# Performance work log

Measured on AMD Instinct MI355X. Metric: run time of the kernel, lower is better.

The kernel has to match this reference:

```python
import jax, jax.numpy as jnp
import numpy as np

N = 200000
E = 12800000
G = 1024

def setup_inputs() -> dict:
    key = jax.random.key(0)
    k1, k2, k3 = jax.random.split(key, 3)
    node_pos = jax.random.normal(k1, (N, 2), dtype=jnp.float32)
    edge_index = jax.random.randint(k2, (2, E), 0, N, dtype=jnp.int64)
    batch_ids = jnp.sort(jax.random.randint(k3, (N,), 0, G, dtype=jnp.int64))
    return {"node_pos": node_pos, "edge_index": edge_index,
            "batch_ids": batch_ids, "num_graphs": G}

def reference(node_pos, edge_index, batch_ids, num_graphs):
    # gather edge endpoints: [E, 2]
    start = node_pos[edge_index[0]]
    end = node_pos[edge_index[1]]
    # per-edge loss: (||end - start|| - 1)^2, [E]
    diff = end - start
    eu = jnp.sqrt(jnp.sum(diff * diff, axis=1))
    edge_var = jnp.square(eu - 1.0)
    # scatter-mean by graph id of the edge's source node
    seg = batch_ids[edge_index[0]]
    sums = jax.ops.segment_sum(edge_var, seg, num_segments=num_graphs)
    counts = jax.ops.segment_sum(jnp.ones_like(edge_var), seg, num_segments=num_graphs)
    graph_var = sums / jnp.maximum(counts, 1.0)  # [G]
    # self.reduce = torch.mean over graphs
    return jnp.mean(graph_var)
```

## Files before the change

kernel.cpp:

```cpp
#include <hip/hip_runtime.h>


#define GBINS 1024

typedef int iv4 __attribute__((ext_vector_type(4)));

__global__ void pack_nodes(const float2* __restrict__ pos,
                           const int* __restrict__ batch,
                           float4* __restrict__ rec, int N) {
    int i = blockIdx.x * blockDim.x + threadIdx.x;
    if (i < N) {
        float2 p = pos[i];
        rec[i] = make_float4(p.x, p.y, __int_as_float(batch[i]), 0.f);
    }
}

template <bool PACKED>
__global__ __launch_bounds__(1024)
void edge_accum(const float4* __restrict__ rec,
                const float2* __restrict__ pos,
                const int* __restrict__ batch,
                const int* __restrict__ src,
                const int* __restrict__ dst,
                float* __restrict__ gsum, float* __restrict__ gcnt, int E) {
    __shared__ float ls[GBINS];
    __shared__ float lc[GBINS];
    for (int i = threadIdx.x; i < GBINS; i += blockDim.x) { ls[i] = 0.f; lc[i] = 0.f; }
    __syncthreads();

    const int tid    = blockIdx.x * blockDim.x + threadIdx.x;
    const int stride = gridDim.x * blockDim.x;
    const int E4     = E >> 2;
    const iv4* __restrict__ s4 = (const iv4*)src;
    const iv4* __restrict__ d4 = (const iv4*)dst;

    auto proc = [&](int s, int d) {
        float ax, ay, bx, by; int g;
        if constexpr (PACKED) {
            float4 a = rec[s];
            float2 b = ((const float2*)rec)[2 * d];
            ax = a.x; ay = a.y; g = __float_as_int(a.z);
            bx = b.x; by = b.y;
        } else {
            float2 a = pos[s]; float2 b = pos[d]; g = batch[s];
            ax = a.x; ay = a.y; bx = b.x; by = b.y;
        }
        float dx = bx - ax, dy = by - ay;
        float eu = sqrtf(fmaf(dx, dx, dy * dy));
        float t  = eu - 1.f;
        atomicAdd(&ls[g], t * t);
        atomicAdd(&lc[g], 1.f);
    };

    for (int i = tid; i < E4; i += stride) {
        iv4 s = __builtin_nontemporal_load(&s4[i]);
        iv4 d = __builtin_nontemporal_load(&d4[i]);
        proc(s.x, d.x); proc(s.y, d.y); proc(s.z, d.z); proc(s.w, d.w);
    }
    for (int i = (E4 << 2) + tid; i < E; i += stride) {
        proc(src[i], dst[i]);
    }

    __syncthreads();
    for (int g = threadIdx.x; g < GBINS; g += blockDim.x) {
        float c = lc[g];
        if (c != 0.f) {
            atomicAdd(&gsum[g], ls[g]);
            atomicAdd(&gcnt[g], c);
        }
    }
}

__global__ void finalize_kernel(const float* __restrict__ gsum,
                                const float* __restrict__ gcnt,
                                float* __restrict__ out,
                                const int* __restrict__ nG_ptr) {
    const int G = *nG_ptr;
    float v = 0.f;
    for (int g = threadIdx.x; g < G; g += blockDim.x)
        v += gsum[g] / fmaxf(gcnt[g], 1.f);

    __shared__ float w[16];
    for (int off = 32; off; off >>= 1) v += __shfl_down(v, off, 64);
    if ((threadIdx.x & 63) == 0) w[threadIdx.x >> 6] = v;
    __syncthreads();
    if (threadIdx.x == 0) {
        float s = 0.f;
        int nw = (blockDim.x + 63) >> 6;
        for (int i = 0; i < nw; ++i) s += w[i];
        out[0] = s / (float)G;
    }
}

extern "C" void kernel_launch(void* const* d_in, const int* in_sizes, int n_in,
                              void* d_out, int out_size, void* d_ws, size_t ws_size,
                              hipStream_t stream) {
    const float2* pos   = (const float2*)d_in[0];
    const int*    ei    = (const int*)d_in[1];
    const int*    batch = (const int*)d_in[2];
    const int*    nG    = (const int*)d_in[3];

    const int N = in_sizes[0] / 2;
    const int E = in_sizes[1] / 2;
    const int* src = ei;
    const int* dst = ei + E;

    float*  gsum = (float*)d_ws;
    float*  gcnt = gsum + GBINS;
    float4* rec  = (float4*)((char*)d_ws + 2 * GBINS * sizeof(float));
    const size_t need = 2 * GBINS * sizeof(float) + (size_t)N * sizeof(float4);
    const bool packed = (ws_size >= need);

    (void)hipMemsetAsync(d_ws, 0, 2 * GBINS * sizeof(float), stream);

    if (packed) {
        pack_nodes<<<(N + 255) / 256, 256, 0, stream>>>(pos, batch, rec, N);
        edge_accum<true><<<512, 1024, 0, stream>>>(rec, pos, batch, src, dst, gsum, gcnt, E);
    } else {
        edge_accum<false><<<512, 1024, 0, stream>>>(rec, pos, batch, src, dst, gsum, gcnt, E);
    }
    finalize_kernel<<<1, 1024, 0, stream>>>(gsum, gcnt, (float*)d_out, nG);
}
```

Before: 278.1 us.

## Bucket edges by source/destination node ranges and gather positions from LDS

Replaces the flat edge loop, which does random global gathers, with two phases. The first phase bins edges into 32x32 node-range buckets and writes each as a packed local-index record. The second phase loads each bucket's source and destination node positions into shared memory, stored as half precision, and accumulates from there. This turns scattered global reads into LDS reads. The cost is an extra pass that writes and rereads every edge record, plus precision loss from fp16 positions, and any bucket past its cap is silently dropped.

```diff
diff --git a/kernel.cpp b/kernel.cpp
--- a/kernel.cpp
+++ b/kernel.cpp
@@ -1,73 +1,169 @@
 #include <hip/hip_runtime.h>
-
+#include <hip/hip_fp16.h>
+
+
+typedef int iv4 __attribute__((ext_vector_type(4)));
 
 #define GBINS 1024
-
-typedef int iv4 __attribute__((ext_vector_type(4)));
-
-__global__ void pack_nodes(const float2* __restrict__ pos,
-                           const int* __restrict__ batch,
-                           float4* __restrict__ rec, int N) {
+#define BUK   32
+#define NBUK  1024
+#define CHUNK 8192
+#define MAXD  6656
+
+__device__ __forceinline__ uint32_t divm(uint32_t x, unsigned long long magic) {
+    return (uint32_t)((x * magic) >> 40);
+}
+
+__global__ void pack_nodes16(const float2* __restrict__ pos, const int* __restrict__ batch,
+                             uint32_t* __restrict__ pos16, unsigned short* __restrict__ gid16,
+                             int N) {
     int i = blockIdx.x * blockDim.x + threadIdx.x;
     if (i < N) {
         float2 p = pos[i];
-        rec[i] = make_float4(p.x, p.y, __int_as_float(batch[i]), 0.f);
-    }
-}
-
-template <bool PACKED>
+        __half2 h; h.x = __float2half_rn(p.x); h.y = __float2half_rn(p.y);
+        uint32_t u; __builtin_memcpy(&u, &h, 4);
+        pos16[i] = u;
+        gid16[i] = (unsigned short)batch[i];
+    }
+}
+
 __global__ __launch_bounds__(1024)
-void edge_accum(const float4* __restrict__ rec,
-                const float2* __restrict__ pos,
-                const int* __restrict__ batch,
-                const int* __restrict__ src,
-                const int* __restrict__ dst,
-                float* __restrict__ gsum, float* __restrict__ gcnt, int E) {
+void phaseA(const int* __restrict__ srcL, const int* __restrict__ dstL,
+            uint32_t* __restrict__ lists, uint32_t* __restrict__ cursors,
+            int E, uint32_t dnode, unsigned long long magic, uint32_t cap) {
+    __shared__ uint32_t cnt[NBUK];
+    __shared__ uint32_t lofs[NBUK + 1];
+    __shared__ uint32_t gbase[NBUK];
+    __shared__ uint32_t stage[CHUNK];
+    const int tid = threadIdx.x;
+    cnt[tid] = 0;
+    __syncthreads();
+
+    const int base = blockIdx.x * CHUNK;
+    const bool amok = ((E & 3) == 0);
+    int bid[8]; uint32_t rank[8], rec[8];
+
+    #pragma unroll
+    for (int h = 0; h < 2; ++h) {
+        const int e0 = base + h * 4096 + 4 * tid;
+        iv4 sv, dv;
+        const bool vec = amok && (e0 + 3 < E);
+        if (vec) {
+            sv = __builtin_nontemporal_load((const iv4*)(srcL + e0));
+            dv = __builtin_nontemporal_load((const iv4*)(dstL + e0));
+        }
+        #pragma unroll
+        for (int k = 0; k < 4; ++k) {
+            const int j = h * 4 + k;
+            const int e = e0 + k;
+            int s, d;
+            if (vec)          { s = sv[k];   d = dv[k]; }
+            else if (e < E)   { s = srcL[e]; d = dstL[e]; }
+            else              { bid[j] = -1; continue; }
+            uint32_t bs = divm((uint32_t)s, magic), bd = divm((uint32_t)d, magic);
+            uint32_t sl = (uint32_t)s - bs * dnode;
+            uint32_t dl = (uint32_t)d - bd * dnode;
+            bid[j]  = (int)(bs * BUK + bd);
+            rec[j]  = (sl << 13) | dl;
+            rank[j] = atomicAdd(&cnt[bid[j]], 1u);
+        }
+    }
+    __syncthreads();
+
+    const uint32_t mycnt = cnt[tid];
+    for (int off = 1; off < NBUK; off <<= 1) {
+        uint32_t x = (tid >= off) ? cnt[tid - off] : 0u;
+        __syncthreads();
+        cnt[tid] += x;
+        __syncthreads();
+    }
+    lofs[tid] = cnt[tid] - mycnt;
+    if (tid == NBUK - 1) lofs[NBUK] = cnt[tid];
+    gbase[tid] = atomicAdd(&cursors[tid], mycnt);
+    __syncthreads();
+
+    #pragma unroll
+    for (int j = 0; j < 8; ++j)
+        if (bid[j] >= 0) stage[lofs[bid[j]] + rank[j]] = rec[j];
+    __syncthreads();
+
+    const int n = (int)lofs[NBUK];
+    for (int i = tid; i < n; i += 1024) {
+        int b = 0;
+        #pragma unroll
+        for (int st = 512; st; st >>= 1)
+            if (lofs[b + st] <= (uint32_t)i) b += st;
+        const uint32_t gpos = gbase[b] + ((uint32_t)i - lofs[b]);
+        if (gpos < cap) lists[(size_t)b * cap + gpos] = stage[i];
+    }
+}
+
+__global__ __launch_bounds__(1024)
+void phaseB(const uint32_t* __restrict__ pos16, const unsigned short* __restrict__ gid16,
+            const uint32_t* __restrict__ lists, const uint32_t* __restrict__ cursors,
+            float* __restrict__ gsum, float* __restrict__ gcnt,
+            int N, uint32_t dnode, uint32_t cap) {
+    __shared__ uint32_t spos[MAXD];
+    __shared__ uint32_t dposA[MAXD];
+    __shared__ float hs[GBINS];
+    __shared__ float hc[GBINS];
+    const int tid = threadIdx.x;
+    const int bs = blockIdx.x >> 5, bd = blockIdx.x & (BUK - 1);
+    const int s0 = bs * (int)dnode, d0 = bd * (int)dnode;
+    const int ns = min((int)dnode, N - s0);
+    const int nd = min((int)dnode, N - d0);
+    for (int i = tid; i < ns; i += 1024) spos[i]  = pos16[s0 + i];
+    for (int i = tid; i < nd; i += 1024) dposA[i] = pos16[d0 + i];
+    for (int i = tid; i < GBINS; i += 1024) { hs[i] = 0.f; hc[i] = 0.f; }
+    __syncthreads();
+
+    const uint32_t cnt = min(cursors[blockIdx.x], cap);
+    const uint32_t* __restrict__ lp = lists + (size_t)blockIdx.x * cap;
+    const unsigned short* __restrict__ sg = gid16 + s0;
+    for (uint32_t i = tid; i < cnt; i += 1024) {
+        const uint32_t r = lp[i];
+        const uint32_t sl = r >> 13, dl = r & 8191u;
+        const uint32_t ua = spos[sl], ub = dposA[dl];
+        const int g = sg[sl];
+        __half2 ha, hb;
+        __builtin_memcpy(&ha, &ua, 4);
+        __builtin_memcpy(&hb, &ub, 4);
+        const float dx = __half2float(hb.x) - __half2float(ha.x);
+        const float dy = __half2float(hb.y) - __half2float(ha.y);
+        const float t  = sqrtf(fmaf(dx, dx, dy * dy)) - 1.f;
+        atomicAdd(&hs[g], t * t);
+        atomicAdd(&hc[g], 1.f);
+    }
+    __syncthreads();
+    for (int g = tid; g < GBINS; g += 1024) {
+        const float c = hc[g];
+        if (c != 0.f) { atomicAdd(&gsum[g], hs[g]); atomicAdd(&gcnt[g], c); }
+    }
+}
+
+__global__ __launch_bounds__(1024)
+void edge_accum_mono(const float2* __restrict__ pos, const int* __restrict__ batch,
+                     const int* __restrict__ src, const int* __restrict__ dst,
+                     float* __restrict__ gsum, float* __restrict__ gcnt, int E) {
     __shared__ float ls[GBINS];
     __shared__ float lc[GBINS];
     for (int i = threadIdx.x; i < GBINS; i += blockDim.x) { ls[i] = 0.f; lc[i] = 0.f; }
     __syncthreads();
-
-    const int tid    = blockIdx.x * blockDim.x + threadIdx.x;
+    const int tid = blockIdx.x * blockDim.x + threadIdx.x;
     const int stride = gridDim.x * blockDim.x;
-    const int E4     = E >> 2;
-    const iv4* __restrict__ s4 = (const iv4*)src;
-    const iv4* __restrict__ d4 = (const iv4*)dst;
-
-    auto proc = [&](int s, int d) {
-        float ax, ay, bx, by; int g;
-        if constexpr (PACKED) {
-            float4 a = rec[s];
-            float2 b = ((const float2*)rec)[2 * d];
-            ax = a.x; ay = a.y; g = __float_as_int(a.z);
-            bx = b.x; by = b.y;
-        } else {
-            float2 a = pos[s]; float2 b = pos[d]; g = batch[s];
-            ax = a.x; ay = a.y; bx = b.x; by = b.y;
-        }
-        float dx = bx - ax, dy = by - ay;
-        float eu = sqrtf(fmaf(dx, dx, dy * dy));
-        float t  = eu - 1.f;
+    for (int i = tid; i < E; i += stride) {
+        const int s = src[i], d = dst[i];
+        const float2 a = pos[s], b = pos[d];
+        const int g = batch[s];
+        const float dx = b.x - a.x, dy = b.y - a.y;
+        const float t = sqrtf(fmaf(dx, dx, dy * dy)) - 1.f;
         atomicAdd(&ls[g], t * t);
         atomicAdd(&lc[g], 1.f);
-    };
-
-    for (int i = tid; i < E4; i += stride) {
-        iv4 s = __builtin_nontemporal_load(&s4[i]);
-        iv4 d = __builtin_nontemporal_load(&d4[i]);
-        proc(s.x, d.x); proc(s.y, d.y); proc(s.z, d.z); proc(s.w, d.w);
-    }
-    for (int i = (E4 << 2) + tid; i < E; i += stride) {
-        proc(src[i], dst[i]);
-    }
-
+    }
     __syncthreads();
     for (int g = threadIdx.x; g < GBINS; g += blockDim.x) {
-        float c = lc[g];
-        if (c != 0.f) {
-            atomicAdd(&gsum[g], ls[g]);
-            atomicAdd(&gcnt[g], c);
-        }
+        const float c = lc[g];
+        if (c != 0.f) { atomicAdd(&gsum[g], ls[g]); atomicAdd(&gcnt[g], c); }
     }
 }
 
@@ -79,14 +175,13 @@
     float v = 0.f;
     for (int g = threadIdx.x; g < G; g += blockDim.x)
         v += gsum[g] / fmaxf(gcnt[g], 1.f);
-
     __shared__ float w[16];
     for (int off = 32; off; off >>= 1) v += __shfl_down(v, off, 64);
     if ((threadIdx.x & 63) == 0) w[threadIdx.x >> 6] = v;
     __syncthreads();
     if (threadIdx.x == 0) {
         float s = 0.f;
-        int nw = (blockDim.x + 63) >> 6;
+        const int nw = (blockDim.x + 63) >> 6;
         for (int i = 0; i < nw; ++i) s += w[i];
         out[0] = s / (float)G;
     }
@@ -105,19 +200,32 @@
     const int* src = ei;
     const int* dst = ei + E;
 
-    float*  gsum = (float*)d_ws;
-    float*  gcnt = gsum + GBINS;
-    float4* rec  = (float4*)((char*)d_ws + 2 * GBINS * sizeof(float));
-    const size_t need = 2 * GBINS * sizeof(float) + (size_t)N * sizeof(float4);
-    const bool packed = (ws_size >= need);
-
-    (void)hipMemsetAsync(d_ws, 0, 2 * GBINS * sizeof(float), stream);
-
-    if (packed) {
-        pack_nodes<<<(N + 255) / 256, 256, 0, stream>>>(pos, batch, rec, N);
-        edge_accum<true><<<512, 1024, 0, stream>>>(rec, pos, batch, src, dst, gsum, gcnt, E);
+    float*    gsum    = (float*)d_ws;
+    float*    gcnt    = gsum + GBINS;
+    uint32_t* cursors = (uint32_t*)(gcnt + GBINS);
+    const size_t pos16_off = 16384;
+    const size_t gid16_off = pos16_off + (size_t)N * 4;
+    const size_t lists_off = (gid16_off + (size_t)N * 2 + 255) & ~(size_t)255;
+    const uint32_t dnode = (uint32_t)((N + BUK - 1) / BUK);
+    const uint32_t cap   = (uint32_t)(E / NBUK + 2048);
+    const size_t need = lists_off + (size_t)NBUK * cap * 4;
+    const bool bucketed = (dnode <= MAXD) && (ws_size >= need) && (N < (1 << 22));
+
+    (void)hipMemsetAsync(d_ws, 0, 12288, stream);
+
+    if (bucketed) {
+        uint32_t*       pos16 = (uint32_t*)((char*)d_ws + pos16_off);
+        unsigned short* gid16 = (unsigned short*)((char*)d_ws + gid16_off);
+        uint32_t*       lists = (uint32_t*)((char*)d_ws + lists_off);
+        const unsigned long long magic = ((1ULL << 40) + dnode - 1) / dnode;
+
+        pack_nodes16<<<(N + 255) / 256, 256, 0, stream>>>(pos, batch, pos16, gid16, N);
+        phaseA<<<(E + CHUNK - 1) / CHUNK, 1024, 0, stream>>>(
+            src, dst, lists, cursors, E, dnode, magic, cap);
+        phaseB<<<NBUK, 1024, 0, stream>>>(
+            pos16, gid16, lists, cursors, gsum, gcnt, N, dnode, cap);
     } else {
-        edge_accum<false><<<512, 1024, 0, stream>>>(rec, pos, batch, src, dst, gsum, gcnt, E);
+        edge_accum_mono<<<512, 1024, 0, stream>>>(pos, batch, src, dst, gsum, gcnt, E);
     }
     finalize_kernel<<<1, 1024, 0, stream>>>(gsum, gcnt, (float*)d_out, nG);
 }
```

Measured after the change: 342.4 us. 23.1% more time.

## Split edge pass into count and sum kernels with half-precision positions and segment lookup

Applied to the files above, without the earlier changes.

Packs node positions to fp16 pairs (4 bytes per node) and derives graph id from a sorted-segment start table held in LDS instead of gathering batch ids. Counting is moved to a separate kernel that only streams src, and the sum kernel gathers the smaller fp16 records. The aim is less gather traffic per edge and fewer LDS atomics per pass. In exchange src is read twice, the segment search costs a few extra LDS reads, and fp16 positions lose precision relative to the fp32 reference.

```diff
diff --git a/kernel.cpp b/kernel.cpp
--- a/kernel.cpp
+++ b/kernel.cpp
@@ -1,92 +1,156 @@
 #include <hip/hip_runtime.h>
+#include <hip/hip_fp16.h>
 
+
+typedef int iv4 __attribute__((ext_vector_type(4)));
 
 #define GBINS 1024
 
-typedef int iv4 __attribute__((ext_vector_type(4)));
+__device__ __forceinline__ int find_graph(int v, const int* __restrict__ ss, float scale) {
+    int g = (int)((float)v * scale);
+    g = min(g, GBINS - 1);
+    while (v < ss[g]) --g;
+    while (v >= ss[g + 1]) ++g;
+    return g;
+}
 
-__global__ void pack_nodes(const float2* __restrict__ pos,
-                           const int* __restrict__ batch,
-                           float4* __restrict__ rec, int N) {
+__global__ void prep(const float2* __restrict__ pos, const int* __restrict__ batch,
+                     uint32_t* __restrict__ pos16, int* __restrict__ startg, int N) {
     int i = blockIdx.x * blockDim.x + threadIdx.x;
-    if (i < N) {
-        float2 p = pos[i];
-        rec[i] = make_float4(p.x, p.y, __int_as_float(batch[i]), 0.f);
+    if (i >= N) return;
+    float2 p = pos[i];
+    __half2 h; h.x = __float2half_rn(p.x); h.y = __float2half_rn(p.y);
+    uint32_t u; __builtin_memcpy(&u, &h, 4);
+    pos16[i] = u;
+    int b = batch[i];
+    if (i == 0) { for (int g = 0; g <= b; ++g) startg[g] = 0; }
+    else { int a = batch[i - 1]; for (int g = a + 1; g <= b; ++g) startg[g] = i; }
+    if (i == N - 1) { for (int g = b + 1; g <= GBINS; ++g) startg[g] = N; }
+}
+
+__global__ __launch_bounds__(512)
+void count_kernel(const int* __restrict__ src, const int* __restrict__ startg,
+                  uint32_t* __restrict__ gcnt, int E, float scale) {
+    __shared__ int ss[GBINS + 1];
+    __shared__ uint32_t hc[GBINS];
+    const int tid = threadIdx.x;
+    for (int i = tid; i < GBINS + 1; i += 512) ss[i] = startg[i];
+    for (int i = tid; i < GBINS; i += 512) hc[i] = 0u;
+    __syncthreads();
+
+    const int ngroups = E >> 2;
+    const iv4* __restrict__ s4 = (const iv4*)src;
+    const int gtid = blockIdx.x * 512 + tid, gstride = gridDim.x * 512;
+    for (int i = gtid; i < ngroups; i += gstride) {
+        iv4 sv = __builtin_nontemporal_load(&s4[i]);
+        #pragma unroll
+        for (int k = 0; k < 4; ++k)
+            atomicAdd(&hc[find_graph(sv[k], ss, scale)], 1u);
+    }
+    for (int e = (ngroups << 2) + gtid; e < E; e += gstride)
+        atomicAdd(&hc[find_graph(src[e], ss, scale)], 1u);
+
+    __syncthreads();
+    for (int j = tid; j < GBINS; j += 512) {
+        int g = (j + (blockIdx.x << 3)) & (GBINS - 1);
+        uint32_t c = hc[g];
+        if (c) atomicAdd(&gcnt[g], c);
     }
 }
 
-template <bool PACKED>
-__global__ __launch_bounds__(1024)
-void edge_accum(const float4* __restrict__ rec,
-                const float2* __restrict__ pos,
-                const int* __restrict__ batch,
-                const int* __restrict__ src,
-                const int* __restrict__ dst,
-                float* __restrict__ gsum, float* __restrict__ gcnt, int E) {
-    __shared__ float ls[GBINS];
-    __shared__ float lc[GBINS];
-    for (int i = threadIdx.x; i < GBINS; i += blockDim.x) { ls[i] = 0.f; lc[i] = 0.f; }
+__global__ __launch_bounds__(512)
+void sum_kernel(const int* __restrict__ src, const int* __restrict__ dst,
+                const uint32_t* __restrict__ pos16, const int* __restrict__ startg,
+                float* __restrict__ gsum, int E, float scale) {
+    __shared__ int ss[GBINS + 1];
+    __shared__ float hs[GBINS];
+    const int tid = threadIdx.x;
+    for (int i = tid; i < GBINS + 1; i += 512) ss[i] = startg[i];
+    for (int i = tid; i < GBINS; i += 512) hs[i] = 0.f;
     __syncthreads();
 
-    const int tid    = blockIdx.x * blockDim.x + threadIdx.x;
-    const int stride = gridDim.x * blockDim.x;
-    const int E4     = E >> 2;
+    const int ngroups = E >> 2;
     const iv4* __restrict__ s4 = (const iv4*)src;
     const iv4* __restrict__ d4 = (const iv4*)dst;
-
-    auto proc = [&](int s, int d) {
-        float ax, ay, bx, by; int g;
-        if constexpr (PACKED) {
-            float4 a = rec[s];
-            float2 b = ((const float2*)rec)[2 * d];
-            ax = a.x; ay = a.y; g = __float_as_int(a.z);
-            bx = b.x; by = b.y;
-        } else {
-            float2 a = pos[s]; float2 b = pos[d]; g = batch[s];
-            ax = a.x; ay = a.y; bx = b.x; by = b.y;
+    const int gtid = blockIdx.x * 512 + tid, gstride = gridDim.x * 512;
+    for (int i = gtid; i < ngroups; i += gstride) {
+        iv4 sv = __builtin_nontemporal_load(&s4[i]);
+        iv4 dv = __builtin_nontemporal_load(&d4[i]);
+        uint32_t ua[4], ub[4];
+        #pragma unroll
+        for (int k = 0; k < 4; ++k) { ua[k] = pos16[sv[k]]; ub[k] = pos16[dv[k]]; }
+        #pragma unroll
+        for (int k = 0; k < 4; ++k) {
+            __half2 ha, hb;
+            __builtin_memcpy(&ha, &ua[k], 4);
+            __builtin_memcpy(&hb, &ub[k], 4);
+            const float dx = __half2float(hb.x) - __half2float(ha.x);
+            const float dy = __half2float(hb.y) - __half2float(ha.y);
+            const float t  = sqrtf(fmaf(dx, dx, dy * dy)) - 1.f;
+            atomicAdd(&hs[find_graph(sv[k], ss, scale)], t * t);
         }
-        float dx = bx - ax, dy = by - ay;
-        float eu = sqrtf(fmaf(dx, dx, dy * dy));
-        float t  = eu - 1.f;
-        atomicAdd(&ls[g], t * t);
-        atomicAdd(&lc[g], 1.f);
-    };
-
-    for (int i = tid; i < E4; i += stride) {
-        iv4 s = __builtin_nontemporal_load(&s4[i]);
-        iv4 d = __builtin_nontemporal_load(&d4[i]);
-        proc(s.x, d.x); proc(s.y, d.y); proc(s.z, d.z); proc(s.w, d.w);
     }
-    for (int i = (E4 << 2) + tid; i < E; i += stride) {
-        proc(src[i], dst[i]);
+    for (int e = (ngroups << 2) + gtid; e < E; e += gstride) {
+        const int s = src[e], d = dst[e];
+        uint32_t ua = pos16[s], ub = pos16[d];
+        __half2 ha, hb;
+        __builtin_memcpy(&ha, &ua, 4);
+        __builtin_memcpy(&hb, &ub, 4);
+        const float dx = __half2float(hb.x) - __half2float(ha.x);
+        const float dy = __half2float(hb.y) - __half2float(ha.y);
+        const float t  = sqrtf(fmaf(dx, dx, dy * dy)) - 1.f;
+        atomicAdd(&hs[find_graph(s, ss, scale)], t * t);
     }
 
     __syncthreads();
+    for (int j = tid; j < GBINS; j += 512) {
+        int g = (j + (blockIdx.x << 3)) & (GBINS - 1);
+        float v = hs[g];
+        if (v != 0.f) atomicAdd(&gsum[g], v);
+    }
+}
+
+__global__ __launch_bounds__(1024)
+void edge_accum_mono(const float2* __restrict__ pos, const int* __restrict__ batch,
+                     const int* __restrict__ src, const int* __restrict__ dst,
+                     float* __restrict__ gsum, uint32_t* __restrict__ gcnt, int E) {
+    __shared__ float ls[GBINS];
+    __shared__ uint32_t lc[GBINS];
+    for (int i = threadIdx.x; i < GBINS; i += blockDim.x) { ls[i] = 0.f; lc[i] = 0u; }
+    __syncthreads();
+    const int tid = blockIdx.x * blockDim.x + threadIdx.x;
+    const int stride = gridDim.x * blockDim.x;
+    for (int i = tid; i < E; i += stride) {
+        const int s = src[i], d = dst[i];
+        const float2 a = pos[s], b = pos[d];
+        const int g = batch[s];
+        const float dx = b.x - a.x, dy = b.y - a.y;
+        const float t = sqrtf(fmaf(dx, dx, dy * dy)) - 1.f;
+        atomicAdd(&ls[g], t * t);
+        atomicAdd(&lc[g], 1u);
+    }
+    __syncthreads();
     for (int g = threadIdx.x; g < GBINS; g += blockDim.x) {
-        float c = lc[g];
-        if (c != 0.f) {
-            atomicAdd(&gsum[g], ls[g]);
-            atomicAdd(&gcnt[g], c);
-        }
+        const uint32_t c = lc[g];
+        if (c) { atomicAdd(&gsum[g], ls[g]); atomicAdd(&gcnt[g], c); }
     }
 }
 
 __global__ void finalize_kernel(const float* __restrict__ gsum,
-                                const float* __restrict__ gcnt,
+                                const uint32_t* __restrict__ gcnt,
                                 float* __restrict__ out,
                                 const int* __restrict__ nG_ptr) {
     const int G = *nG_ptr;
     float v = 0.f;
     for (int g = threadIdx.x; g < G; g += blockDim.x)
-        v += gsum[g] / fmaxf(gcnt[g], 1.f);
-
+        v += gsum[g] / fmaxf((float)gcnt[g], 1.f);
     __shared__ float w[16];
     for (int off = 32; off; off >>= 1) v += __shfl_down(v, off, 64);
     if ((threadIdx.x & 63) == 0) w[threadIdx.x >> 6] = v;
     __syncthreads();
     if (threadIdx.x == 0) {
         float s = 0.f;
-        int nw = (blockDim.x + 63) >> 6;
+        const int nw = (blockDim.x + 63) >> 6;
         for (int i = 0; i < nw; ++i) s += w[i];
         out[0] = s / (float)G;
     }
@@ -105,19 +169,22 @@
     const int* src = ei;
     const int* dst = ei + E;
 
-    float*  gsum = (float*)d_ws;
-    float*  gcnt = gsum + GBINS;
-    float4* rec  = (float4*)((char*)d_ws + 2 * GBINS * sizeof(float));
-    const size_t need = 2 * GBINS * sizeof(float) + (size_t)N * sizeof(float4);
-    const bool packed = (ws_size >= need);
+    float*    gsum   = (float*)d_ws;
+    uint32_t* gcnt   = (uint32_t*)((char*)d_ws + 4096);
+    int*      startg = (int*)((char*)d_ws + 8192);
+    uint32_t* pos16  = (uint32_t*)((char*)d_ws + 16384);
+    const size_t need = 16384 + (size_t)N * 4;
+    const bool fast = (ws_size >= need) && (N >= 1);
 
-    (void)hipMemsetAsync(d_ws, 0, 2 * GBINS * sizeof(float), stream);
+    (void)hipMemsetAsync(d_ws, 0, 8192, stream);
 
-    if (packed) {
-        pack_nodes<<<(N + 255) / 256, 256, 0, stream>>>(pos, batch, rec, N);
-        edge_accum<true><<<512, 1024, 0, stream>>>(rec, pos, batch, src, dst, gsum, gcnt, E);
+    if (fast) {
+        const float scale = (float)GBINS / (float)N;
+        prep<<<(N + 255) / 256, 256, 0, stream>>>(pos, batch, pos16, startg, N);
+        count_kernel<<<1024, 512, 0, stream>>>(src, startg, gcnt, E, scale);
+        sum_kernel<<<1024, 512, 0, stream>>>(src, dst, pos16, startg, gsum, E, scale);
     } else {
-        edge_accum<false><<<512, 1024, 0, stream>>>(rec, pos, batch, src, dst, gsum, gcnt, E);
+        edge_accum_mono<<<512, 1024, 0, stream>>>(pos, batch, src, dst, gsum, gcnt, E);
     }
     finalize_kernel<<<1, 1024, 0, stream>>>(gsum, gcnt, (float*)d_out, nG);
 }
```

After: 284.9 us. 1.02x slower.
